# Kernel optimization log

Measured on AMD Instinct MI355X. Metric: run time of the kernel, lower is better.

## Reference

```python
import jax, jax.numpy as jnp
import numpy as np


def apply_rotary_emb(x, freqs_cis):
    # x: [B, N, H, Dh], freqs_cis: [N, Dh//2, 2]
    B, N, H, Dh = x.shape
    x2 = x.reshape(B, N, H, Dh // 2, 2)
    f = freqs_cis[None, :, None]  # [1, N, 1, Dh//2, 2]
    real = x2[..., 0] * f[..., 0] - x2[..., 1] * f[..., 1]
    imag = x2[..., 1] * f[..., 0] + x2[..., 0] * f[..., 1]
    out = jnp.stack([real, imag], axis=-1)
    return out.reshape(B, N, H, Dh).astype(x.dtype)


def setup_inputs() -> dict:
    key = jax.random.key(0)
    k1, k2, k3, k4 = jax.random.split(key, 4)
    B, N, dim, n_head = 2, 2048, 2048, 16
    head_dim = dim // n_head
    x = jax.random.normal(k1, (B, N, dim), dtype=jnp.float32)
    # realistic rotary freqs (cos/sin), though random also works for correctness
    pos = jnp.arange(N, dtype=jnp.float32)[:, None]
    inv_freq = 1.0 / (10000.0 ** (jnp.arange(0, head_dim, 2, dtype=jnp.float32) / head_dim))
    ang = pos * inv_freq[None, :]  # [N, Dh//2]
    freqs_cis = jnp.stack([jnp.cos(ang), jnp.sin(ang)], axis=-1)  # [N, Dh//2, 2]
    wqkv = jax.random.normal(k2, (dim, 3 * dim), dtype=jnp.float32) * (dim ** -0.5)
    wo = jax.random.normal(k3, (dim, dim), dtype=jnp.float32) * (dim ** -0.5)
    return {"x": x, "freqs_cis": freqs_cis, "wqkv": wqkv, "wo": wo}


def reference(x, freqs_cis, wqkv, wo):
    B, N, dim = x.shape
    n_head = 16
    head_dim = dim // n_head
    qkv = x @ wqkv  # [B, N, 3*dim]
    q, k, v = jnp.split(qkv, 3, axis=-1)
    q = q.reshape(B, N, n_head, head_dim)
    k = k.reshape(B, N, n_head, head_dim)
    v = v.reshape(B, N, n_head, head_dim)
    q = apply_rotary_emb(q, freqs_cis)
    k = apply_rotary_emb(k, freqs_cis)
    scale = 1.0 / jnp.sqrt(jnp.asarray(head_dim, dtype=q.dtype))
    scores = jnp.einsum('bqhd,bkhd->bhqk', q, k) * scale
    attn = jax.nn.softmax(scores, axis=-1)
    out = jnp.einsum('bhqk,bkhd->bqhd', attn, v).reshape(B, N, dim)
    return out @ wo
```

## Files before the change

kernel.cpp:

```cpp
#include <hip/hip_runtime.h>
#include <hip/hip_bf16.h>
#include <stdint.h>

typedef __attribute__((ext_vector_type(8))) short bf16x8;
typedef __attribute__((ext_vector_type(4))) float f32x4;
typedef __attribute__((ext_vector_type(4))) unsigned short u16x4;
typedef __attribute__((ext_vector_type(8))) unsigned short u16x8;

#define DEV __device__ __forceinline__

DEV unsigned short f2bf(float f) {
  union { __hip_bfloat16 h; unsigned short u; } cv;
  cv.h = __float2bfloat16(f);
  return cv.u;
}

DEV void gload_lds16(const void* g, void* l) {
  __builtin_amdgcn_global_load_lds(
      (__attribute__((address_space(1))) void*)(uintptr_t)g,
      (__attribute__((address_space(3))) void*)(uint32_t)(uintptr_t)l,
      16, 0, 0);
}

__global__ __launch_bounds__(256) void k_convert(const float* __restrict__ in,
                                                 unsigned short* __restrict__ out,
                                                 int n8) {
  int i = blockIdx.x * 256 + threadIdx.x;
  if (i >= n8) return;
  const float4* p = (const float4*)in + (size_t)i * 2;
  float4 a = p[0], b = p[1];
  u16x8 o;
  o[0] = f2bf(a.x); o[1] = f2bf(a.y); o[2] = f2bf(a.z); o[3] = f2bf(a.w);
  o[4] = f2bf(b.x); o[5] = f2bf(b.y); o[6] = f2bf(b.z); o[7] = f2bf(b.w);
  *((u16x8*)out + (size_t)i) = o;
}

__global__ __launch_bounds__(256) void k_transpose_bf16(const float* __restrict__ in,
                                                        unsigned short* __restrict__ out,
                                                        int R, int C) {
  __shared__ float tile[32][33];
  const int t = threadIdx.x;
  const int c0 = blockIdx.x * 32, r0 = blockIdx.y * 32;
  {
    int r = t >> 3, c4 = (t & 7) * 4;
    float4 v = *(const float4*)&in[(size_t)(r0 + r) * C + c0 + c4];
    tile[r][c4] = v.x; tile[r][c4 + 1] = v.y; tile[r][c4 + 2] = v.z; tile[r][c4 + 3] = v.w;
  }
  __syncthreads();
  int c = t >> 3, r4 = (t & 7) * 4;
  u16x4 o;
  o[0] = f2bf(tile[r4 + 0][c]); o[1] = f2bf(tile[r4 + 1][c]);
  o[2] = f2bf(tile[r4 + 2][c]); o[3] = f2bf(tile[r4 + 3][c]);
  *(u16x4*)&out[(size_t)(c0 + c) * R + r0 + r4] = o;
}

__global__ __launch_bounds__(512, 2) void k_gemm_qkv(
    const unsigned short* __restrict__ A,
    const unsigned short* __restrict__ Bt,
    unsigned short* __restrict__ qb,
    unsigned short* __restrict__ kb,
    unsigned short* __restrict__ vt,
    const float* __restrict__ freqs) {
  constexpr int Kdim = 2048;
  __shared__ unsigned short As[2][16384];
  __shared__ unsigned short Bs[2][16384];
  const int t = threadIdx.x;
  const int lane = t & 63, wid = t >> 6;
  const int l15 = lane & 15, l4 = (lane >> 4) & 3;
  const int wm = wid >> 2, wn = wid & 3;
  const int bid = blockIdx.x;
  const int wg = (bid & 7) * 48 + (bid >> 3);
  const int by = wg & 15, bx = wg >> 4;
  const int m0 = by * 256, n0 = bx * 256;

  f32x4 acc[8][4];
#pragma unroll
  for (int i = 0; i < 8; i++)
#pragma unroll
    for (int j = 0; j < 4; j++) acc[i][j] = (f32x4)0.f;

  auto stageU = [&](unsigned short* dstUnit, const unsigned short* src, int khalf) {
#pragma unroll
    for (int cb = 0; cb < 2; cb++) {
      int slotu = cb * 512 + wid * 64;
      int slot = slotu + lane;
      int row = slot >> 2, ch = slot & 3;
      gload_lds16(src + (size_t)row * Kdim + khalf * 32 + ch * 8,
                  dstUnit + slotu * 8);
    }
  };

  auto rdA2 = [&](int buf, int kk, int mh, bf16x8 (&f)[4]) {
    const unsigned short* base = &As[buf][kk * 8192];
#pragma unroll
    for (int mi = 0; mi < 4; mi++) {
      int row = wm * 128 + mh * 64 + mi * 16 + l15;
      f[mi] = *(const bf16x8*)&base[row * 32 + l4 * 8];
    }
  };
  auto rdB2 = [&](int buf, int kk, bf16x8 (&f)[4]) {
    const unsigned short* base = &Bs[buf][kk * 8192];
#pragma unroll
    for (int ni = 0; ni < 4; ni++) {
      int row = wn * 64 + ni * 16 + l15;
      f[ni] = *(const bf16x8*)&base[row * 32 + l4 * 8];
    }
  };
  auto mmaP = [&](bf16x8 (&a4)[4], bf16x8 (&b4)[4], int mib) {
    __builtin_amdgcn_s_setprio(1);
#pragma unroll
    for (int mi = 0; mi < 4; mi++)
#pragma unroll
      for (int ni = 0; ni < 4; ni++)
        acc[mib + mi][ni] = __builtin_amdgcn_mfma_f32_16x16x32_bf16(
            a4[mi], b4[ni], acc[mib + mi][ni], 0, 0, 0);
    __builtin_amdgcn_s_setprio(0);
  };

  const unsigned short* Abase = A + (size_t)m0 * Kdim;
  const unsigned short* Bbase = Bt + (size_t)n0 * Kdim;

  stageU(&As[0][0], Abase, 0);
  stageU(&Bs[0][0], Bbase, 0);
  stageU(&As[0][8192], Abase, 1);
  stageU(&Bs[0][8192], Bbase, 1);
  asm volatile("s_waitcnt vmcnt(4)" ::: "memory");
  __builtin_amdgcn_s_barrier();

  bf16x8 a4[4], b4[4];
  for (int j = 0; j < 32; j++) {
    const int buf = j & 1;
    const unsigned short* An = Abase + (j + 1) * 64;
    const unsigned short* Bn = Bbase + (j + 1) * 64;
    unsigned short* Ad = &As[buf ^ 1][0];
    unsigned short* Bd = &Bs[buf ^ 1][0];
    const bool st = (j < 31);

    rdA2(buf, 0, 0, a4);
    rdB2(buf, 0, b4);
    if (st) stageU(Ad, An, 0);
    __builtin_amdgcn_s_barrier();
    asm volatile("s_waitcnt lgkmcnt(0)" ::: "memory");
    __builtin_amdgcn_sched_barrier(0);
    mmaP(a4, b4, 0);
    __builtin_amdgcn_s_barrier();

    rdA2(buf, 0, 1, a4);
    if (st) stageU(Bd, Bn, 0);
    __builtin_amdgcn_s_barrier();
    asm volatile("s_waitcnt lgkmcnt(0)" ::: "memory");
    __builtin_amdgcn_sched_barrier(0);
    mmaP(a4, b4, 4);
    asm volatile("s_waitcnt vmcnt(4)" ::: "memory");
    __builtin_amdgcn_s_barrier();

    rdA2(buf, 1, 0, a4);
    rdB2(buf, 1, b4);
    if (st) stageU(Ad + 8192, An, 1);
    __builtin_amdgcn_s_barrier();
    asm volatile("s_waitcnt lgkmcnt(0)" ::: "memory");
    __builtin_amdgcn_sched_barrier(0);
    mmaP(a4, b4, 0);
    __builtin_amdgcn_s_barrier();

    rdA2(buf, 1, 1, a4);
    if (st) stageU(Bd + 8192, Bn, 1);
    __builtin_amdgcn_s_barrier();
    asm volatile("s_waitcnt lgkmcnt(0)" ::: "memory");
    __builtin_amdgcn_sched_barrier(0);
    mmaP(a4, b4, 4);
    asm volatile("s_waitcnt vmcnt(4)" ::: "memory");
    __builtin_amdgcn_s_barrier();
  }

#pragma unroll
  for (int mi = 0; mi < 8; mi++) {
    int rowb = m0 + wm * 128 + mi * 16 + l4 * 4;
    int b = rowb >> 11;
    int tok0 = rowb & 2047;
#pragma unroll
    for (int ni = 0; ni < 4; ni++) {
      int col = n0 + wn * 64 + ni * 16 + l15;
      int sec = col >> 11;
      int h = (col >> 7) & 15;
      int dh = col & 127;
      if (sec == 2) {
        u16x4 o;
#pragma unroll
        for (int r = 0; r < 4; r++) o[r] = f2bf(acc[mi][ni][r]);
        *(u16x4*)&vt[((size_t)(b * 16 + h) * 128 + dh) * 2048 + tok0] = o;
      } else {
        unsigned short* dst = (sec == 0) ? qb : kb;
        int dh2 = dh >> 1;
        int odd = dh & 1;
#pragma unroll
        for (int r = 0; r < 4; r++) {
          float v = acc[mi][ni][r];
          float p = __shfl_xor(v, 1, 64);
          float2 cs = *(const float2*)&freqs[((size_t)(tok0 + r) * 64 + dh2) * 2];
          float o = odd ? (v * cs.x + p * cs.y) : (v * cs.x - p * cs.y);
          dst[((size_t)(b * 16 + h) * 2048 + tok0 + r) * 128 + dh] = f2bf(o);
        }
      }
    }
  }
}

__global__ __launch_bounds__(256) void k_gemm_out(
    const unsigned short* __restrict__ A,
    const unsigned short* __restrict__ Bt,
    int Kdim, int Nn,
    float* __restrict__ Cout) {
  __shared__ unsigned short As[128 * 64];
  __shared__ unsigned short Bs[128 * 64];
  const int t = threadIdx.x;
  const int lane = t & 63, wid = t >> 6;
  const int l15 = lane & 15, l4 = lane >> 4;
  const int m0 = blockIdx.y * 128, n0 = blockIdx.x * 128;
  const int wr = (wid >> 1) * 64, wc = (wid & 1) * 64;

  f32x4 acc[4][4];
#pragma unroll
  for (int i = 0; i < 4; i++)
#pragma unroll
    for (int j = 0; j < 4; j++) acc[i][j] = (f32x4)0.f;

  for (int k0 = 0; k0 < Kdim; k0 += 64) {
    __syncthreads();
#pragma unroll
    for (int j = 0; j < 4; j++) {
      int slotbase = j * 256 + wid * 64;
      int slot = slotbase + lane;
      int row = slot >> 3, cc = slot & 7;
      int cg = cc ^ (row & 7);
      gload_lds16(A + (size_t)(m0 + row) * Kdim + k0 + cg * 8, &As[slotbase * 8]);
      gload_lds16(Bt + (size_t)(n0 + row) * Kdim + k0 + cg * 8, &Bs[slotbase * 8]);
    }
    __syncthreads();
#pragma unroll
    for (int kk = 0; kk < 2; kk++) {
      bf16x8 af[4], bfr[4];
#pragma unroll
      for (int mi = 0; mi < 4; mi++) {
        int row = wr + mi * 16 + l15;
        int c = (kk * 4 + l4) ^ (row & 7);
        af[mi] = *(const bf16x8*)&As[row * 64 + c * 8];
      }
#pragma unroll
      for (int ni = 0; ni < 4; ni++) {
        int row = wc + ni * 16 + l15;
        int c = (kk * 4 + l4) ^ (row & 7);
        bfr[ni] = *(const bf16x8*)&Bs[row * 64 + c * 8];
      }
#pragma unroll
      for (int mi = 0; mi < 4; mi++)
#pragma unroll
        for (int ni = 0; ni < 4; ni++)
          acc[mi][ni] = __builtin_amdgcn_mfma_f32_16x16x32_bf16(af[mi], bfr[ni],
                                                                acc[mi][ni], 0, 0, 0);
    }
  }

#pragma unroll
  for (int mi = 0; mi < 4; mi++) {
    int rowb = m0 + wr + mi * 16 + l4 * 4;
#pragma unroll
    for (int ni = 0; ni < 4; ni++) {
      int col = n0 + wc + ni * 16 + l15;
#pragma unroll
      for (int r = 0; r < 4; r++)
        Cout[(size_t)(rowb + r) * Nn + col] = acc[mi][ni][r];
    }
  }
}

__global__ __launch_bounds__(256, 2) void k_attn(
    const unsigned short* __restrict__ qb,
    const unsigned short* __restrict__ kb,
    const unsigned short* __restrict__ vt,
    unsigned short* __restrict__ ao) {
  __shared__ unsigned short Ks[2][64 * 128];
  __shared__ unsigned short Vs[2][64 * 128];
  __shared__ unsigned short Ps[4][32 * 64];
  const int t = threadIdx.x;
  const int lane = t & 63, wid = t >> 6;
  const int l15 = lane & 15, l4 = lane >> 4;
  const int qt0 = blockIdx.x * 128;
  const int bh = blockIdx.y;
  const unsigned short* qbase = qb + (size_t)bh * 2048 * 128;
  const unsigned short* kbase = kb + (size_t)bh * 2048 * 128;
  const unsigned short* vbase = vt + (size_t)bh * 128 * 2048;

  bf16x8 qf[2][4];
#pragma unroll
  for (int mi = 0; mi < 2; mi++) {
    int qrow = qt0 + wid * 32 + mi * 16 + l15;
#pragma unroll
    for (int dk = 0; dk < 4; dk++)
      qf[mi][dk] = *(const bf16x8*)&qbase[(size_t)qrow * 128 + dk * 32 + l4 * 8];
  }

  f32x4 O[2][8];
#pragma unroll
  for (int mi = 0; mi < 2; mi++)
#pragma unroll
    for (int df = 0; df < 8; df++) O[mi][df] = (f32x4)0.f;
  float lsum[2][4];
#pragma unroll
  for (int mi = 0; mi < 2; mi++)
#pragma unroll
    for (int r = 0; r < 4; r++) lsum[mi][r] = 0.f;

  const float scale = 0.08838834764831845f;

  auto STAGE = [&](int kv0, int buf) {
#pragma unroll
    for (int j = 0; j < 4; j++) {
      int slotbase = j * 256 + wid * 64;
      int slot = slotbase + lane;
      int rowk = slot >> 4, ck = slot & 15;
      gload_lds16(&kbase[(size_t)(kv0 + rowk) * 128 + (ck ^ (rowk & 7)) * 8],
                  &Ks[buf][slotbase * 8]);
      int rowv = slot >> 3, cv = slot & 7;
      gload_lds16(&vbase[(size_t)rowv * 2048 + kv0 + (cv ^ (rowv & 7)) * 8],
                  &Vs[buf][slotbase * 8]);
    }
  };

  STAGE(0, 0);
  __syncthreads();

  for (int ti = 0; ti < 32; ti++) {
    const int cur = ti & 1;
    if (ti < 31) STAGE((ti + 1) * 64, cur ^ 1);

    f32x4 s[2][4];
#pragma unroll
    for (int mi = 0; mi < 2; mi++)
#pragma unroll
      for (int ni = 0; ni < 4; ni++) s[mi][ni] = (f32x4)0.f;
#pragma unroll
    for (int dk = 0; dk < 4; dk++) {
      bf16x8 kf[4];
#pragma unroll
      for (int ni = 0; ni < 4; ni++) {
        int row = ni * 16 + l15;
        int c = (dk * 4 + l4) ^ (row & 7);
        kf[ni] = *(const bf16x8*)&Ks[cur][row * 128 + c * 8];
      }
#pragma unroll
      for (int mi = 0; mi < 2; mi++)
#pragma unroll
        for (int ni = 0; ni < 4; ni++)
          s[mi][ni] = __builtin_amdgcn_mfma_f32_16x16x32_bf16(qf[mi][dk], kf[ni],
                                                              s[mi][ni], 0, 0, 0);
    }

    unsigned short* pbase = &Ps[wid][0];
#pragma unroll
    for (int mi = 0; mi < 2; mi++)
#pragma unroll
      for (int ni = 0; ni < 4; ni++) {
        int col = ni * 16 + l15;
#pragma unroll
        for (int r = 0; r < 4; r++) {
          float p = __expf(s[mi][ni][r] * scale);
          lsum[mi][r] += p;
          int rowp = mi * 16 + l4 * 4 + r;
          pbase[rowp * 64 + (((col >> 3) ^ (rowp & 7)) << 3) + (col & 7)] = f2bf(p);
        }
      }

    bf16x8 pf[2][2];
#pragma unroll
    for (int mi = 0; mi < 2; mi++)
#pragma unroll
      for (int kk = 0; kk < 2; kk++) {
        int row = mi * 16 + l15;
        int c = (kk * 4 + l4) ^ (row & 7);
        pf[mi][kk] = *(const bf16x8*)&pbase[row * 64 + c * 8];
      }

#pragma unroll
    for (int df = 0; df < 8; df++) {
      bf16x8 vf[2];
#pragma unroll
      for (int kk = 0; kk < 2; kk++) {
        int row = df * 16 + l15;
        int c = (kk * 4 + l4) ^ (row & 7);
        vf[kk] = *(const bf16x8*)&Vs[cur][row * 64 + c * 8];
      }
#pragma unroll
      for (int mi = 0; mi < 2; mi++)
#pragma unroll
        for (int kk = 0; kk < 2; kk++)
          O[mi][df] = __builtin_amdgcn_mfma_f32_16x16x32_bf16(pf[mi][kk], vf[kk],
                                                              O[mi][df], 0, 0, 0);
    }

    __syncthreads();
  }

  float inv[2][4];
#pragma unroll
  for (int mi = 0; mi < 2; mi++)
#pragma unroll
    for (int r = 0; r < 4; r++) {
      float v = lsum[mi][r];
      v += __shfl_xor(v, 1, 64);
      v += __shfl_xor(v, 2, 64);
      v += __shfl_xor(v, 4, 64);
      v += __shfl_xor(v, 8, 64);
      inv[mi][r] = 1.0f / v;
    }

  const int b = bh >> 4, h = bh & 15;
#pragma unroll
  for (int mi = 0; mi < 2; mi++)
#pragma unroll
    for (int df = 0; df < 8; df++)
#pragma unroll
      for (int r = 0; r < 4; r++) {
        int tok = qt0 + wid * 32 + mi * 16 + l4 * 4 + r;
        ao[((size_t)(b * 2048 + tok)) * 2048 + h * 128 + df * 16 + l15] =
            f2bf(O[mi][df][r] * inv[mi][r]);
      }
}

extern "C" void kernel_launch(void* const* d_in, const int* in_sizes, int n_in,
                              void* d_out, int out_size, void* d_ws, size_t ws_size,
                              hipStream_t stream) {
  const float* x     = (const float*)d_in[0];
  const float* freqs = (const float*)d_in[1];
  const float* wqkv  = (const float*)d_in[2];
  const float* wo    = (const float*)d_in[3];
  float* out = (float*)d_out;

  char* ws = (char*)d_ws;
  unsigned short* xb    = (unsigned short*)(ws + 0);
  unsigned short* wqkvT = (unsigned short*)(ws + 16777216);
  unsigned short* woT   = (unsigned short*)(ws + 41943040);
  unsigned short* qb    = (unsigned short*)(ws + 50331648);
  unsigned short* kb    = (unsigned short*)(ws + 67108864);
  unsigned short* vt    = (unsigned short*)(ws + 83886080);
  unsigned short* ao    = (unsigned short*)(ws + 100663296);

  k_convert<<<dim3(4096), dim3(256), 0, stream>>>(x, xb, 1048576);
  k_transpose_bf16<<<dim3(192, 64), dim3(256), 0, stream>>>(wqkv, wqkvT, 2048, 6144);
  k_transpose_bf16<<<dim3(64, 64), dim3(256), 0, stream>>>(wo, woT, 2048, 2048);

  k_gemm_qkv<<<dim3(384), dim3(512), 0, stream>>>(xb, wqkvT, qb, kb, vt, freqs);

  k_attn<<<dim3(16, 32), dim3(256), 0, stream>>>(qb, kb, vt, ao);

  k_gemm_out<<<dim3(16, 32), dim3(256), 0, stream>>>(ao, woT, 2048, 2048, out);
}
```

Baseline: 287.9 us.

## Swizzle LDS tiles and deepen QKV GEMM prefetch pipeline

Applies an XOR swizzle to the 16-byte chunk index when staging A/B tiles into LDS and when reading MFMA fragments, to reduce LDS bank conflicts on the 64-byte row stride. It also restructures the k-loop so that loads are issued further ahead: the next half-tile is staged early and the k-tile two steps ahead is loaded into the freed half of the current buffer, with vmcnt waits raised to keep more loads in flight. This aims to hide global latency better, at the cost of more complex wait accounting where a wrong count would race.

```diff
diff --git a/kernel.cpp b/kernel.cpp
--- a/kernel.cpp
+++ b/kernel.cpp
@@ -84,8 +84,9 @@
     for (int cb = 0; cb < 2; cb++) {
       int slotu = cb * 512 + wid * 64;
       int slot = slotu + lane;
-      int row = slot >> 2, ch = slot & 3;
-      gload_lds16(src + (size_t)row * Kdim + khalf * 32 + ch * 8,
+      int row = slot >> 2, s = slot & 3;
+      int c = s ^ ((row >> 1) & 3);
+      gload_lds16(src + (size_t)row * Kdim + khalf * 32 + c * 8,
                   dstUnit + slotu * 8);
     }
   };
@@ -95,7 +96,8 @@
 #pragma unroll
     for (int mi = 0; mi < 4; mi++) {
       int row = wm * 128 + mh * 64 + mi * 16 + l15;
-      f[mi] = *(const bf16x8*)&base[row * 32 + l4 * 8];
+      int s = l4 ^ ((row >> 1) & 3);
+      f[mi] = *(const bf16x8*)&base[row * 32 + s * 8];
     }
   };
   auto rdB2 = [&](int buf, int kk, bf16x8 (&f)[4]) {
@@ -103,7 +105,8 @@
 #pragma unroll
     for (int ni = 0; ni < 4; ni++) {
       int row = wn * 64 + ni * 16 + l15;
-      f[ni] = *(const bf16x8*)&base[row * 32 + l4 * 8];
+      int s = l4 ^ ((row >> 1) & 3);
+      f[ni] = *(const bf16x8*)&base[row * 32 + s * 8];
     }
   };
   auto mmaP = [&](bf16x8 (&a4)[4], bf16x8 (&b4)[4], int mib) {
@@ -124,21 +127,21 @@
   stageU(&Bs[0][0], Bbase, 0);
   stageU(&As[0][8192], Abase, 1);
   stageU(&Bs[0][8192], Bbase, 1);
-  asm volatile("s_waitcnt vmcnt(4)" ::: "memory");
+  stageU(&As[1][0], Abase + 64, 0);
+  stageU(&Bs[1][0], Bbase + 64, 0);
+  asm volatile("s_waitcnt vmcnt(8)" ::: "memory");
   __builtin_amdgcn_s_barrier();
 
   bf16x8 a4[4], b4[4];
   for (int j = 0; j < 32; j++) {
     const int buf = j & 1;
-    const unsigned short* An = Abase + (j + 1) * 64;
-    const unsigned short* Bn = Bbase + (j + 1) * 64;
-    unsigned short* Ad = &As[buf ^ 1][0];
-    unsigned short* Bd = &Bs[buf ^ 1][0];
-    const bool st = (j < 31);
 
     rdA2(buf, 0, 0, a4);
     rdB2(buf, 0, b4);
-    if (st) stageU(Ad, An, 0);
+    if (j + 1 < 32) {
+      stageU(&As[buf ^ 1][8192], Abase + (j + 1) * 64, 1);
+      stageU(&Bs[buf ^ 1][8192], Bbase + (j + 1) * 64, 1);
+    }
     __builtin_amdgcn_s_barrier();
     asm volatile("s_waitcnt lgkmcnt(0)" ::: "memory");
     __builtin_amdgcn_sched_barrier(0);
@@ -146,17 +149,20 @@
     __builtin_amdgcn_s_barrier();
 
     rdA2(buf, 0, 1, a4);
-    if (st) stageU(Bd, Bn, 0);
     __builtin_amdgcn_s_barrier();
     asm volatile("s_waitcnt lgkmcnt(0)" ::: "memory");
     __builtin_amdgcn_sched_barrier(0);
     mmaP(a4, b4, 4);
-    asm volatile("s_waitcnt vmcnt(4)" ::: "memory");
+    if (j < 31) asm volatile("s_waitcnt vmcnt(8)" ::: "memory");
+    else        asm volatile("s_waitcnt vmcnt(0)" ::: "memory");
     __builtin_amdgcn_s_barrier();
 
     rdA2(buf, 1, 0, a4);
     rdB2(buf, 1, b4);
-    if (st) stageU(Ad + 8192, An, 1);
+    if (j + 2 < 32) {
+      stageU(&As[buf][0], Abase + (j + 2) * 64, 0);
+      stageU(&Bs[buf][0], Bbase + (j + 2) * 64, 0);
+    }
     __builtin_amdgcn_s_barrier();
     asm volatile("s_waitcnt lgkmcnt(0)" ::: "memory");
     __builtin_amdgcn_sched_barrier(0);
@@ -164,12 +170,12 @@
     __builtin_amdgcn_s_barrier();
 
     rdA2(buf, 1, 1, a4);
-    if (st) stageU(Bd + 8192, Bn, 1);
     __builtin_amdgcn_s_barrier();
     asm volatile("s_waitcnt lgkmcnt(0)" ::: "memory");
     __builtin_amdgcn_sched_barrier(0);
     mmaP(a4, b4, 4);
-    asm volatile("s_waitcnt vmcnt(4)" ::: "memory");
+    if (j < 30)       asm volatile("s_waitcnt vmcnt(8)" ::: "memory");
+    else if (j == 30) asm volatile("s_waitcnt vmcnt(4)" ::: "memory");
     __builtin_amdgcn_s_barrier();
   }
 
```

After: 285.7 us. Within noise of the previous version (-0.8%).
